# Kernel optimization log

Hardware: AMD Instinct MI355X
Metric: run time of the kernel (lower is better)

The kernel has to match this reference:

```python
import jax, jax.numpy as jnp
import numpy as np

DIM = 2048
NUM_HEADS = 16
HEAD_DIM = DIM // NUM_HEADS
SCALE = 1.0 / float(np.sqrt(HEAD_DIM))


def setup_inputs() -> dict:
    key = jax.random.key(0)
    ks = jax.random.split(key, 7)
    B, L = 2, 2048
    x = jax.random.normal(ks[0], (B, L, DIM), dtype=jnp.float32)
    s = 1.0 / np.sqrt(DIM)
    # nn.Linear stores weight as [out, in]; y = x @ W.T + b
    Wq = jax.random.uniform(ks[1], (DIM, DIM), jnp.float32, -s, s)
    bq = jax.random.uniform(ks[2], (DIM,), jnp.float32, -s, s)
    Wk = jax.random.uniform(ks[3], (DIM, DIM), jnp.float32, -s, s)
    bk = jax.random.uniform(ks[4], (DIM,), jnp.float32, -s, s)
    Wv = jax.random.uniform(ks[5], (DIM, DIM), jnp.float32, -s, s)
    bv = jax.random.uniform(ks[6], (DIM,), jnp.float32, -s, s)
    return {"x": x, "Wq": Wq, "bq": bq, "Wk": Wk, "bk": bk, "Wv": Wv, "bv": bv}


def _attn(x, Wq, bq, Wk, bk, Wv, bv):
    B, L, D = x.shape
    H, Hd = NUM_HEADS, HEAD_DIM
    # projections: x @ W.T + b, then split heads -> [B, H, L, Hd]
    q = (x @ Wq.T + bq).reshape(B, L, H, Hd).transpose(0, 2, 1, 3)
    k = (x @ Wk.T + bk).reshape(B, L, H, Hd).transpose(0, 2, 1, 3)
    v = (x @ Wv.T + bv).reshape(B, L, H, Hd).transpose(0, 2, 1, 3)
    scores = jnp.einsum("bhqd,bhkd->bhqk", q, k) * SCALE  # [B,H,L,L]
    attn = jax.nn.softmax(scores, axis=-1)
    out = jnp.einsum("bhqk,bhkd->bhqd", attn, v)
    return out.transpose(0, 2, 1, 3).reshape(B, L, D)


def reference(x, Wq, bq, Wk, bk, Wv, bv):
    return _attn(x, Wq, bq, Wk, bk, Wv, bv)
```

## Files before the change

kernel.cpp:

```cpp
#include <hip/hip_runtime.h>
#include <stdint.h>

typedef unsigned short u16;
typedef __attribute__((ext_vector_type(8))) short short8;
typedef __attribute__((ext_vector_type(16))) float f32x16;

#define ATTN_SCALE 0.08838834764831845f

__device__ __forceinline__ u16 f2bf(float f) {
  union { float f; uint32_t u; } a; a.f = f;
  return (u16)((a.u + 0x7fffu + ((a.u >> 16) & 1u)) >> 16);
}

__device__ __forceinline__ void async16(const u16* g, u16* lds) {
  __builtin_amdgcn_global_load_lds(
      (const __attribute__((address_space(1))) void*)g,
      (__attribute__((address_space(3))) void*)lds, 16, 0, 0);
}

__global__ void cvt_kernel(const float* __restrict__ src, u16* __restrict__ dst, int n8) {
  int i = blockIdx.x * 256 + threadIdx.x;
  if (i >= n8) return;
  const float4* s4 = (const float4*)src;
  float4 a = s4[2 * i], c = s4[2 * i + 1];
  union { u16 h[8]; uint4 v; } o;
  o.h[0] = f2bf(a.x); o.h[1] = f2bf(a.y); o.h[2] = f2bf(a.z); o.h[3] = f2bf(a.w);
  o.h[4] = f2bf(c.x); o.h[5] = f2bf(c.y); o.h[6] = f2bf(c.z); o.h[7] = f2bf(c.w);
  ((uint4*)dst)[i] = o.v;
}

__global__ void cvtw_kernel(const float* __restrict__ w0, const float* __restrict__ w1,
                            const float* __restrict__ w2, u16* __restrict__ dst) {
  int z = blockIdx.y;
  const float* src = (z == 0) ? w0 : (z == 1) ? w1 : w2;
  int i = blockIdx.x * 256 + threadIdx.x;
  const float4* s4 = (const float4*)src;
  float4 a = s4[2 * i], c = s4[2 * i + 1];
  union { u16 h[8]; uint4 v; } o;
  o.h[0] = f2bf(a.x); o.h[1] = f2bf(a.y); o.h[2] = f2bf(a.z); o.h[3] = f2bf(a.w);
  o.h[4] = f2bf(c.x); o.h[5] = f2bf(c.y); o.h[6] = f2bf(c.z); o.h[7] = f2bf(c.w);
  ((uint4*)(dst + (size_t)z * 4194304))[i] = o.v;
}

__global__ __launch_bounds__(256, 3) void qkv_gemm(
    const u16* __restrict__ xb, const u16* __restrict__ Wb,
    const float* __restrict__ bq, const float* __restrict__ bk, const float* __restrict__ bv,
    u16* __restrict__ qkv) {
  __shared__ __align__(16) u16 As[2][128 * 32];
  __shared__ __align__(16) u16 Bs[2][128 * 32];
  const int z = blockIdx.z;
  const int n0 = blockIdx.x * 128, m0 = blockIdx.y * 128;
  const u16* Bw = Wb + (size_t)z * (2048u * 2048u);
  const float* bias = (z == 0) ? bq : (z == 1) ? bk : bv;
  u16* dst = qkv + (size_t)z * 8388608u;
  const int t = threadIdx.x, wave = t >> 6, lane = t & 63;
  const int wm = wave >> 1, wn = wave & 1, l31 = lane & 31, h = lane >> 5;

  const int cid0 = wave * 128 + lane;
  f32x16 acc[2][2];
#pragma unroll
  for (int i = 0; i < 2; ++i)
#pragma unroll
    for (int j = 0; j < 2; ++j)
#pragma unroll
      for (int r = 0; r < 16; ++r) acc[i][j][r] = 0.f;

#pragma unroll 1
  for (int n = 0; n < 64; ++n) {
    if (n == 0) {
#pragma unroll
      for (int p = 0; p < 2; ++p) {
        const int cid = cid0 + p * 64, row = cid >> 2, col = (cid & 3) * 8;
        async16(xb + (size_t)(m0 + row) * 2048 + col, &As[0][cid * 8]);
        async16(Bw + (size_t)(n0 + row) * 2048 + col, &Bs[0][cid * 8]);
      }
    }
    __syncthreads();
    const int cur = n & 1;
    if (n + 1 < 64) {
      const int k1 = (n + 1) * 32;
#pragma unroll
      for (int p = 0; p < 2; ++p) {
        const int cid = cid0 + p * 64, row = cid >> 2, col = (cid & 3) * 8;
        async16(xb + (size_t)(m0 + row) * 2048 + k1 + col, &As[cur ^ 1][cid * 8]);
        async16(Bw + (size_t)(n0 + row) * 2048 + k1 + col, &Bs[cur ^ 1][cid * 8]);
      }
    }
#pragma unroll
    for (int ks = 0; ks < 2; ++ks) {
      short8 af[2], bf[2];
#pragma unroll
      for (int i = 0; i < 2; ++i)
        af[i] = *(const short8*)&As[cur][(wm * 64 + i * 32 + l31) * 32 + ks * 16 + h * 8];
#pragma unroll
      for (int j = 0; j < 2; ++j)
        bf[j] = *(const short8*)&Bs[cur][(wn * 64 + j * 32 + l31) * 32 + ks * 16 + h * 8];
#pragma unroll
      for (int i = 0; i < 2; ++i)
#pragma unroll
        for (int j = 0; j < 2; ++j)
          acc[i][j] = __builtin_amdgcn_mfma_f32_32x32x16_bf16(af[i], bf[j], acc[i][j], 0, 0, 0);
    }
  }

#pragma unroll
  for (int j = 0; j < 2; ++j) {
    const int col = n0 + wn * 64 + j * 32 + l31;
    const float bb_ = bias[col];
    const int hh = col >> 7, hd = col & 127;
#pragma unroll
    for (int i = 0; i < 2; ++i) {
#pragma unroll
      for (int g = 0; g < 4; ++g) {
        const int lbase = m0 + wm * 64 + i * 32 + 8 * g + 4 * h;
        const int bb = lbase >> 11, l0 = lbase & 2047;
        if (z == 2) {
          union { u16 q[4]; ushort2 d[2]; } pk;
#pragma unroll
          for (int rr = 0; rr < 4; ++rr) pk.q[rr] = f2bf(acc[i][j][4 * g + rr] + bb_);
          *(uint2*)&dst[((size_t)(bb * 16 + hh) * 128 + hd) * 2048 + l0] = *(uint2*)pk.q;
        } else {
#pragma unroll
          for (int rr = 0; rr < 4; ++rr)
            dst[((size_t)(bb * 16 + hh) * 2048 + (l0 + rr)) * 128 + hd] =
                f2bf(acc[i][j][4 * g + rr] + bb_);
        }
      }
    }
  }
}

__global__ __launch_bounds__(256, 2) void attn_kernel(
    const u16* __restrict__ Qg,
    const u16* __restrict__ Kg,
    const u16* __restrict__ Vtg,
    float* __restrict__ out) {
  __shared__ __align__(16) u16 Ks[2][64 * 128];
  __shared__ __align__(16) u16 Vs[2][128 * 64];
  const int bh = blockIdx.y, q0 = blockIdx.x * 128;
  const int t = threadIdx.x, wave = t >> 6, lane = t & 63;
  const int l31 = lane & 31, h = lane >> 5;
  const u16* Qp = Qg + (size_t)bh * 262144;
  const u16* Kp = Kg + (size_t)bh * 262144;
  const u16* Vp = Vtg + (size_t)bh * 262144;
  const int b = bh >> 4, hd = bh & 15;
  const int qrow = q0 + wave * 32 + l31;

  short8 qf[8];
#pragma unroll
  for (int s = 0; s < 8; ++s)
    qf[s] = *(const short8*)&Qp[(size_t)qrow * 128 + s * 16 + h * 8];

  f32x16 oac[4];
#pragma unroll
  for (int dt = 0; dt < 4; ++dt)
#pragma unroll
    for (int r = 0; r < 16; ++r) oac[dt][r] = 0.f;
  float den = 0.f;
  const int cidK = wave * 256 + lane;

#pragma unroll 1
  for (int n = 0; n < 32; ++n) {
    if (n == 0) {
#pragma unroll
      for (int p = 0; p < 4; ++p) {
        const int cid = cidK + p * 64;
        const int rk = cid >> 4, gk = (cid & 15) ^ (rk & 15);
        async16(Kp + (size_t)rk * 128 + gk * 8, &Ks[0][cid * 8]);
        const int rv = cid >> 3, gv = (cid & 7) ^ (rv & 7);
        async16(Vp + (size_t)rv * 2048 + gv * 8, &Vs[0][cid * 8]);
      }
    }
    __syncthreads();
    const int cur = n & 1;
    if (n + 1 < 32) {
      const int k1 = (n + 1) * 64;
#pragma unroll
      for (int p = 0; p < 4; ++p) {
        const int cid = cidK + p * 64;
        const int rk = cid >> 4, gk = (cid & 15) ^ (rk & 15);
        async16(Kp + (size_t)(k1 + rk) * 128 + gk * 8, &Ks[cur ^ 1][cid * 8]);
        const int rv = cid >> 3, gv = (cid & 7) ^ (rv & 7);
        async16(Vp + (size_t)rv * 2048 + k1 + gv * 8, &Vs[cur ^ 1][cid * 8]);
      }
    }

#pragma unroll
    for (int T = 0; T < 2; ++T) {
      const int krow = T * 32 + l31;
      f32x16 sc;
#pragma unroll
      for (int r = 0; r < 16; ++r) sc[r] = 0.f;
#pragma unroll
      for (int s = 0; s < 8; ++s) {
        const short8 kf = *(const short8*)&Ks[cur][(krow * 16 + (((2 * s + h) ^ (krow & 15)))) * 8];
        sc = __builtin_amdgcn_mfma_f32_32x32x16_bf16(kf, qf[s], sc, 0, 0, 0);
      }
      uint32_t pp[8];
#pragma unroll
      for (int i = 0; i < 8; ++i) {
        const float e0 = __expf(fminf(sc[2 * i] * ATTN_SCALE, 80.f));
        const float e1 = __expf(fminf(sc[2 * i + 1] * ATTN_SCALE, 80.f));
        den += e0 + e1;
        union { float f; uint32_t u; } u0, u1; u0.f = e0; u1.f = e1;
        pp[i] = ((u1.u + 0x8000u) & 0xffff0000u) | ((u0.u + 0x8000u) >> 16);
      }
      uint32_t x[8];
#pragma unroll
      for (int i = 0; i < 8; ++i) x[i] = __shfl_xor(pp[i], 32, 64);
#pragma unroll
      for (int ks = 0; ks < 2; ++ks) {
        const int o0 = ks * 4;
        union { uint32_t u[4]; short8 s8; } bfp;
        bfp.u[0] = h ? x[o0 + 2] : pp[o0 + 0];
        bfp.u[1] = h ? x[o0 + 3] : pp[o0 + 1];
        bfp.u[2] = h ? pp[o0 + 2] : x[o0 + 0];
        bfp.u[3] = h ? pp[o0 + 3] : x[o0 + 1];
        const int gk = T * 4 + ks * 2 + h;
#pragma unroll
        for (int dt = 0; dt < 4; ++dt) {
          const int vrow = dt * 32 + l31;
          const short8 vf = *(const short8*)&Vs[cur][(vrow * 8 + (gk ^ (vrow & 7))) * 8];
          oac[dt] = __builtin_amdgcn_mfma_f32_32x32x16_bf16(vf, bfp.s8, oac[dt], 0, 0, 0);
        }
      }
    }
  }

  den += __shfl_xor(den, 32, 64);
  const float inv = 1.f / den;
#pragma unroll
  for (int dt = 0; dt < 4; ++dt) {
#pragma unroll
    for (int g4 = 0; g4 < 4; ++g4) {
      float4 o;
      o.x = oac[dt][4 * g4 + 0] * inv;
      o.y = oac[dt][4 * g4 + 1] * inv;
      o.z = oac[dt][4 * g4 + 2] * inv;
      o.w = oac[dt][4 * g4 + 3] * inv;
      const int d = dt * 32 + g4 * 8 + h * 4;
      *(float4*)&out[((size_t)(b * 2048 + qrow)) * 2048 + hd * 128 + d] = o;
    }
  }
}

extern "C" void kernel_launch(void* const* d_in, const int* in_sizes, int n_in,
                              void* d_out, int out_size, void* d_ws, size_t ws_size,
                              hipStream_t stream) {
  const float* x  = (const float*)d_in[0];
  const float* Wq = (const float*)d_in[1];
  const float* bq = (const float*)d_in[2];
  const float* Wk = (const float*)d_in[3];
  const float* bk = (const float*)d_in[4];
  const float* Wv = (const float*)d_in[5];
  const float* bv = (const float*)d_in[6];
  float* out = (float*)d_out;
  if (ws_size < 92274688u) return;

  u16* xb  = (u16*)d_ws;
  u16* Wb  = xb + 8388608;
  u16* qkv = Wb + 12582912;

  cvt_kernel<<<4096, 256, 0, stream>>>(x, xb, 1048576);
  cvtw_kernel<<<dim3(2048, 3), 256, 0, stream>>>(Wq, Wk, Wv, Wb);
  qkv_gemm<<<dim3(16, 32, 3), 256, 0, stream>>>(xb, Wb, bq, bk, bv, qkv);
  attn_kernel<<<dim3(16, 32), 256, 0, stream>>>(qkv, qkv + 8388608, qkv + 16777216, out);
}
```

Baseline: 366.0 us.

## Swizzle GEMM LDS layout, single-buffer attention tiles, raise occupancy bounds

The QKV GEMM now loads tiles into LDS with an XOR-swizzled layout and precomputed per-thread offsets, so fragment reads avoid bank conflicts, and its launch bound rises to 4 blocks per CU. The attention kernel drops double buffering of K/V tiles in favour of a single buffer filled synchronously each iteration. This halves its LDS footprint so 3 blocks per CU can be resident. The trade is that attention loses load/compute overlap within a block and relies on more resident blocks to hide latency, while tighter register limits may cause spills.

```diff
diff --git a/kernel.cpp b/kernel.cpp
--- a/kernel.cpp
+++ b/kernel.cpp
@@ -42,7 +42,7 @@
   ((uint4*)(dst + (size_t)z * 4194304))[i] = o.v;
 }
 
-__global__ __launch_bounds__(256, 3) void qkv_gemm(
+__global__ __launch_bounds__(256, 4) void qkv_gemm(
     const u16* __restrict__ xb, const u16* __restrict__ Wb,
     const float* __restrict__ bq, const float* __restrict__ bk, const float* __restrict__ bv,
     u16* __restrict__ qkv) {
@@ -56,7 +56,24 @@
   const int t = threadIdx.x, wave = t >> 6, lane = t & 63;
   const int wm = wave >> 1, wn = wave & 1, l31 = lane & 31, h = lane >> 5;
 
-  const int cid0 = wave * 128 + lane;
+  int soff[2], goff[2];
+#pragma unroll
+  for (int p = 0; p < 2; ++p) {
+    const int s = p * 256 + wave * 64 + lane;
+    const int R = s >> 4, j = s & 15, u = j ^ (R & 15);
+    const int m = R * 4 + (u >> 2), c = u & 3;
+    soff[p] = s * 8;
+    goff[p] = m * 2048 + c * 8;
+  }
+  int fr16[2][2], fR15[2][2];
+  const int q4 = (l31 & 3) * 4;
+#pragma unroll
+  for (int i = 0; i < 2; ++i) {
+    const int mA = wm * 64 + i * 32 + l31, mB = wn * 64 + i * 32 + l31;
+    fr16[0][i] = (mA >> 2) * 16; fR15[0][i] = (mA >> 2) & 15;
+    fr16[1][i] = (mB >> 2) * 16; fR15[1][i] = (mB >> 2) & 15;
+  }
+
   f32x16 acc[2][2];
 #pragma unroll
   for (int i = 0; i < 2; ++i)
@@ -64,15 +81,17 @@
     for (int j = 0; j < 2; ++j)
 #pragma unroll
       for (int r = 0; r < 16; ++r) acc[i][j][r] = 0.f;
+
+  const u16* Abase = xb + (size_t)m0 * 2048;
+  const u16* Bbase = Bw + (size_t)n0 * 2048;
 
 #pragma unroll 1
   for (int n = 0; n < 64; ++n) {
     if (n == 0) {
 #pragma unroll
       for (int p = 0; p < 2; ++p) {
-        const int cid = cid0 + p * 64, row = cid >> 2, col = (cid & 3) * 8;
-        async16(xb + (size_t)(m0 + row) * 2048 + col, &As[0][cid * 8]);
-        async16(Bw + (size_t)(n0 + row) * 2048 + col, &Bs[0][cid * 8]);
+        async16(Abase + goff[p], &As[0][soff[p]]);
+        async16(Bbase + goff[p], &Bs[0][soff[p]]);
       }
     }
     __syncthreads();
@@ -81,20 +100,19 @@
       const int k1 = (n + 1) * 32;
 #pragma unroll
       for (int p = 0; p < 2; ++p) {
-        const int cid = cid0 + p * 64, row = cid >> 2, col = (cid & 3) * 8;
-        async16(xb + (size_t)(m0 + row) * 2048 + k1 + col, &As[cur ^ 1][cid * 8]);
-        async16(Bw + (size_t)(n0 + row) * 2048 + k1 + col, &Bs[cur ^ 1][cid * 8]);
+        async16(Abase + goff[p] + k1, &As[cur ^ 1][soff[p]]);
+        async16(Bbase + goff[p] + k1, &Bs[cur ^ 1][soff[p]]);
       }
     }
 #pragma unroll
     for (int ks = 0; ks < 2; ++ks) {
+      const int c = ks * 2 + h;
       short8 af[2], bf[2];
 #pragma unroll
-      for (int i = 0; i < 2; ++i)
-        af[i] = *(const short8*)&As[cur][(wm * 64 + i * 32 + l31) * 32 + ks * 16 + h * 8];
-#pragma unroll
-      for (int j = 0; j < 2; ++j)
-        bf[j] = *(const short8*)&Bs[cur][(wn * 64 + j * 32 + l31) * 32 + ks * 16 + h * 8];
+      for (int i = 0; i < 2; ++i) {
+        af[i] = *(const short8*)&As[cur][(fr16[0][i] + ((q4 + c) ^ fR15[0][i])) * 8];
+        bf[i] = *(const short8*)&Bs[cur][(fr16[1][i] + ((q4 + c) ^ fR15[1][i])) * 8];
+      }
 #pragma unroll
       for (int i = 0; i < 2; ++i)
 #pragma unroll
@@ -115,10 +133,10 @@
         const int lbase = m0 + wm * 64 + i * 32 + 8 * g + 4 * h;
         const int bb = lbase >> 11, l0 = lbase & 2047;
         if (z == 2) {
-          union { u16 q[4]; ushort2 d[2]; } pk;
+          union { u16 q[4]; uint2 d; } pk;
 #pragma unroll
           for (int rr = 0; rr < 4; ++rr) pk.q[rr] = f2bf(acc[i][j][4 * g + rr] + bb_);
-          *(uint2*)&dst[((size_t)(bb * 16 + hh) * 128 + hd) * 2048 + l0] = *(uint2*)pk.q;
+          *(uint2*)&dst[((size_t)(bb * 16 + hh) * 128 + hd) * 2048 + l0] = pk.d;
         } else {
 #pragma unroll
           for (int rr = 0; rr < 4; ++rr)
@@ -130,13 +148,13 @@
   }
 }
 
-__global__ __launch_bounds__(256, 2) void attn_kernel(
+__global__ __launch_bounds__(256, 3) void attn_kernel(
     const u16* __restrict__ Qg,
     const u16* __restrict__ Kg,
     const u16* __restrict__ Vtg,
     float* __restrict__ out) {
-  __shared__ __align__(16) u16 Ks[2][64 * 128];
-  __shared__ __align__(16) u16 Vs[2][128 * 64];
+  __shared__ __align__(16) u16 Ks[64 * 128];
+  __shared__ __align__(16) u16 Vs[128 * 64];
   const int bh = blockIdx.y, q0 = blockIdx.x * 128;
   const int t = threadIdx.x, wave = t >> 6, lane = t & 63;
   const int l31 = lane & 31, h = lane >> 5;
@@ -151,39 +169,32 @@
   for (int s = 0; s < 8; ++s)
     qf[s] = *(const short8*)&Qp[(size_t)qrow * 128 + s * 16 + h * 8];
 
+  int kOff[4], kSlot[4], vOff[4], vSlot[4];
+#pragma unroll
+  for (int p = 0; p < 4; ++p) {
+    const int s = p * 256 + wave * 64 + lane;
+    const int rk = s >> 4, gk = (s & 15) ^ (rk & 15);
+    kSlot[p] = s * 8; kOff[p] = rk * 128 + gk * 8;
+    const int rv = s >> 3, gv = (s & 7) ^ (rv & 7);
+    vSlot[p] = s * 8; vOff[p] = rv * 2048 + gv * 8;
+  }
+
   f32x16 oac[4];
 #pragma unroll
   for (int dt = 0; dt < 4; ++dt)
 #pragma unroll
     for (int r = 0; r < 16; ++r) oac[dt][r] = 0.f;
   float den = 0.f;
-  const int cidK = wave * 256 + lane;
 
 #pragma unroll 1
-  for (int n = 0; n < 32; ++n) {
-    if (n == 0) {
-#pragma unroll
-      for (int p = 0; p < 4; ++p) {
-        const int cid = cidK + p * 64;
-        const int rk = cid >> 4, gk = (cid & 15) ^ (rk & 15);
-        async16(Kp + (size_t)rk * 128 + gk * 8, &Ks[0][cid * 8]);
-        const int rv = cid >> 3, gv = (cid & 7) ^ (rv & 7);
-        async16(Vp + (size_t)rv * 2048 + gv * 8, &Vs[0][cid * 8]);
-      }
-    }
+  for (int kt = 0; kt < 32; ++kt) {
+    const int k0 = kt * 64;
     __syncthreads();
-    const int cur = n & 1;
-    if (n + 1 < 32) {
-      const int k1 = (n + 1) * 64;
-#pragma unroll
-      for (int p = 0; p < 4; ++p) {
-        const int cid = cidK + p * 64;
-        const int rk = cid >> 4, gk = (cid & 15) ^ (rk & 15);
-        async16(Kp + (size_t)(k1 + rk) * 128 + gk * 8, &Ks[cur ^ 1][cid * 8]);
-        const int rv = cid >> 3, gv = (cid & 7) ^ (rv & 7);
-        async16(Vp + (size_t)rv * 2048 + k1 + gv * 8, &Vs[cur ^ 1][cid * 8]);
-      }
-    }
+#pragma unroll
+    for (int p = 0; p < 4; ++p) async16(Kp + (size_t)k0 * 128 + kOff[p], &Ks[kSlot[p]]);
+#pragma unroll
+    for (int p = 0; p < 4; ++p) async16(Vp + (size_t)k0 + vOff[p], &Vs[vSlot[p]]);
+    __syncthreads();
 
 #pragma unroll
     for (int T = 0; T < 2; ++T) {
@@ -193,7 +204,7 @@
       for (int r = 0; r < 16; ++r) sc[r] = 0.f;
 #pragma unroll
       for (int s = 0; s < 8; ++s) {
-        const short8 kf = *(const short8*)&Ks[cur][(krow * 16 + (((2 * s + h) ^ (krow & 15)))) * 8];
+        const short8 kf = *(const short8*)&Ks[(krow * 16 + ((2 * s + h) ^ (krow & 15))) * 8];
         sc = __builtin_amdgcn_mfma_f32_32x32x16_bf16(kf, qf[s], sc, 0, 0, 0);
       }
       uint32_t pp[8];
@@ -220,7 +231,7 @@
 #pragma unroll
         for (int dt = 0; dt < 4; ++dt) {
           const int vrow = dt * 32 + l31;
-          const short8 vf = *(const short8*)&Vs[cur][(vrow * 8 + (gk ^ (vrow & 7))) * 8];
+          const short8 vf = *(const short8*)&Vs[(vrow * 8 + (gk ^ (vrow & 7))) * 8];
           oac[dt] = __builtin_amdgcn_mfma_f32_32x32x16_bf16(vf, bfp.s8, oac[dt], 0, 0, 0);
         }
       }
```

New measurement: 351.4 us. 1.04x faster.
